# Performance work log

Measured on AMD Instinct MI355X. Metric: run time of the kernel, lower is better.

## Reference

```python
import jax, jax.numpy as jnp
import numpy as np


def setup_inputs() -> dict:
    key = jax.random.key(0)
    ks = jax.random.split(key, 6)
    B, S, D = 2, 2048, 1024
    E, DFF = 8, 2048  # E includes always-on expert 0; router sees E-1 routed experts
    scale = 0.02
    return {
        "hidden_states": jax.random.normal(ks[0], (B, S, D), dtype=jnp.float32),
        "router_w": jax.random.normal(ks[1], (D, E - 1), dtype=jnp.float32) * scale,
        "router_b": jnp.zeros((E - 1,), dtype=jnp.float32),
        "wg": jax.random.normal(ks[2], (E, D, DFF), dtype=jnp.float32) * scale,
        "wu": jax.random.normal(ks[3], (E, D, DFF), dtype=jnp.float32) * scale,
        "wd": jax.random.normal(ks[4], (E, DFF, D), dtype=jnp.float32) * scale,
        "top_k": 2,
    }


def _expert_mlp(x, wg_e, wu_e, wd_e):
    # SwiGLU MLP: down( silu(x @ gate) * (x @ up) )
    return (jax.nn.silu(x @ wg_e) * (x @ wu_e)) @ wd_e


def reference(hidden_states, router_w, router_b, wg, wu, wd, top_k):
    B, S, D = hidden_states.shape
    E = wg.shape[0]  # total experts incl. always-on expert 0
    x = hidden_states.reshape(-1, D)  # [T, D]
    T = x.shape[0]

    # Router over E-1 routed experts, softmax in float32
    router_logits = x @ router_w + router_b  # [T, E-1]
    probs = jax.nn.softmax(router_logits.astype(jnp.float32), axis=-1)
    topw, topi = jax.lax.top_k(probs, top_k)  # [T, k]
    topw = topw / jnp.sum(topw, axis=-1, keepdims=True)
    topw = topw.astype(x.dtype)

    # Dense combine weights over routed experts (0 for unselected)
    cw = jnp.zeros((T, E - 1), dtype=x.dtype)
    cw = cw.at[jnp.arange(T)[:, None], topi].add(topw)  # [T, E-1]

    # Always-on expert 0 with weight 1
    out = _expert_mlp(x, wg[0], wu[0], wd[0])  # [T, D]

    # Routed experts 1..E-1 (static small loop over experts)
    for e in range(1, E):
        ye = _expert_mlp(x, wg[e], wu[e], wd[e])  # [T, D]
        out = out + cw[:, e - 1, None] * ye

    return out.reshape(B, S, -1)
```

## Files before the change

kernel.cpp:

```cpp
#include <hip/hip_runtime.h>

#define T_TOK 4096
#define DIM   1024
#define DFF   2048
#define NE    8
#define NR    7
#define MAXNB 71
#define NY    (32 + MAXNB)

typedef __bf16 bf16x8 __attribute__((ext_vector_type(8)));
typedef float  floatx4 __attribute__((ext_vector_type(4)));

__device__ __forceinline__ unsigned short f32_bf16(float f) {
  union { float f; unsigned int u; } v; v.f = f;
  unsigned int u = v.u;
  unsigned int r = (u + 0x7FFFu + ((u >> 16) & 1u)) >> 16;
  return (unsigned short)r;
}

typedef __attribute__((address_space(3))) void lds_void_t;
typedef const __attribute__((address_space(1))) void g_void_t;

__device__ __forceinline__ void gld16(const void* g, void* l) {
  __builtin_amdgcn_global_load_lds((g_void_t*)g, (lds_void_t*)l, 16, 0, 0);
}

__global__ __launch_bounds__(256) void cvt_x_kernel(const float4* __restrict__ in,
                                                    ushort4* __restrict__ out) {
  int i = blockIdx.x * 256 + threadIdx.x;
  float4 v = in[i];
  ushort4 o;
  o.x = f32_bf16(v.x); o.y = f32_bf16(v.y);
  o.z = f32_bf16(v.z); o.w = f32_bf16(v.w);
  out[i] = o;
}

__global__ __launch_bounds__(256) void router_kernel(const float* __restrict__ x,
                                                     const float* __restrict__ rw,
                                                     const float* __restrict__ rb,
                                                     int* __restrict__ idxR,
                                                     float* __restrict__ wslR,
                                                     int* __restrict__ cnt,
                                                     int4* __restrict__ tokE,
                                                     float2* __restrict__ tokW) {
  const int lane = threadIdx.x & 63;
  const int t = blockIdx.x * 4 + (threadIdx.x >> 6);
  const float* xr = x + (size_t)t * DIM;
  float acc[NR];
#pragma unroll
  for (int e = 0; e < NR; e++) acc[e] = 0.f;
  for (int d = lane; d < DIM; d += 64) {
    float xv = xr[d];
#pragma unroll
    for (int e = 0; e < NR; e++) acc[e] += xv * rw[d * NR + e];
  }
#pragma unroll
  for (int off = 32; off > 0; off >>= 1) {
#pragma unroll
    for (int e = 0; e < NR; e++) acc[e] += __shfl_xor(acc[e], off, 64);
  }
  if (lane == 0) {
    float lg[NR];
    float m = -1e30f;
#pragma unroll
    for (int e = 0; e < NR; e++) { lg[e] = acc[e] + rb[e]; m = fmaxf(m, lg[e]); }
    float p[NR], s = 0.f;
#pragma unroll
    for (int e = 0; e < NR; e++) { p[e] = expf(lg[e] - m); s += p[e]; }
#pragma unroll
    for (int e = 0; e < NR; e++) p[e] /= s;
    int i1 = 0;
#pragma unroll
    for (int e = 1; e < NR; e++) if (p[e] > p[i1]) i1 = e;
    int i2 = (i1 == 0) ? 1 : 0;
#pragma unroll
    for (int e = 0; e < NR; e++) if (e != i1 && p[e] > p[i2]) i2 = e;
    float w1 = p[i1], w2 = p[i2], sw = w1 + w2;
    float w1n = w1 / sw, w2n = w2 / sw;
    int s1 = atomicAdd(&cnt[i1], 1);
    idxR[i1 * 4096 + s1] = t; wslR[i1 * 4096 + s1] = w1n;
    int s2 = atomicAdd(&cnt[i2], 1);
    idxR[i2 * 4096 + s2] = t; wslR[i2 * 4096 + s2] = w2n;
    int4 te; te.x = i1; te.y = s1; te.z = i2; te.w = s2;
    tokE[t] = te;
    float2 tw; tw.x = w1n; tw.y = w2n;
    tokW[t] = tw;
  }
}

__global__ __launch_bounds__(256) void sched_kernel(const int* __restrict__ cnt,
                                                    int* __restrict__ idxR,
                                                    float* __restrict__ wslR,
                                                    int4* __restrict__ schedAll,
                                                    int4* __restrict__ schedP,
                                                    int* __restrict__ prefOut,
                                                    int rsb) {
  __shared__ int nb[NR], pref[NR];
  if (threadIdx.x == 0) {
    int p = 0;
    for (int e = 0; e < NR; e++) { int c = cnt[e]; int n = (c + 127) >> 7; nb[e] = n; pref[e] = p; p += n; }
  }
  __syncthreads();
  if (threadIdx.x < NR) prefOut[threadIdx.x] = pref[threadIdx.x];
  for (int e = 0; e < NR; e++) {
    int c = cnt[e], top = nb[e] * 128;
    for (int i = c + (int)threadIdx.x; i < top; i += 256) {
      idxR[e * 4096 + i] = 0; wslR[e * 4096 + i] = 0.f;
    }
  }
  const int NBtot = pref[NR - 1] + nb[NR - 1];
  for (int y = threadIdx.x; y < 32; y += 256) {
    int4 ent; ent.x = 0; ent.y = -1; ent.z = y * 128; ent.w = 0;
    schedAll[y] = ent;
  }
  for (int y = threadIdx.x; y < MAXNB; y += 256) {
    int4 ent; ent.x = -1; ent.y = 0; ent.z = 0; ent.w = 0;
    if (y < NBtot) {
#pragma unroll
      for (int e = 0; e < NR; e++)
        if (y >= pref[e] && y < pref[e] + nb[e]) {
          int rb2 = y - pref[e];
          ent.x = e + 1; ent.y = e * 4096 + rb2 * 128; ent.z = rsb + y * 128;
        }
    }
    schedAll[32 + y] = ent;
  }
  for (int i = threadIdx.x; i < NR * 32; i += 256) {
    int e = i >> 5, rb2 = i & 31;
    int4 ent; ent.w = 0;
    if (rb2 < nb[e]) { ent.x = e + 1; ent.y = e * 4096 + rb2 * 128; ent.z = rb2 * 128; }
    else             { ent.x = -1; ent.y = 0; ent.z = 0; }
    schedP[i] = ent;
  }
}

__global__ __launch_bounds__(256) void transpose_cvt_kernel(
    const float* __restrict__ wg, const float* __restrict__ wu, const float* __restrict__ wd,
    unsigned short* __restrict__ wgt, unsigned short* __restrict__ wut,
    unsigned short* __restrict__ wdt) {
  __shared__ float tile[64][33];
  const int z = blockIdx.z;
  const float* src; unsigned short* dst; int R, C;
  if (z < 8)       { src = wg + (size_t)z * DIM * DFF;        dst = wgt + (size_t)z * DIM * DFF;        R = DIM; C = DFF; }
  else if (z < 16) { src = wu + (size_t)(z - 8) * DIM * DFF;  dst = wut + (size_t)(z - 8) * DIM * DFF;  R = DIM; C = DFF; }
  else             { src = wd + (size_t)(z - 16) * DFF * DIM; dst = wdt + (size_t)(z - 16) * DFF * DIM; R = DFF; C = DIM; }
  const int c0 = blockIdx.x * 32, r0 = blockIdx.y * 64;
  if (c0 >= C || r0 >= R) return;
  const int tx = threadIdx.x & 31, ty = threadIdx.x >> 5;
#pragma unroll
  for (int j = ty; j < 64; j += 8)
    tile[j][tx] = src[(size_t)(r0 + j) * C + c0 + tx];
  __syncthreads();
#pragma unroll
  for (int j = ty; j < 32; j += 8) {
    unsigned int lo = f32_bf16(tile[2 * tx][j]);
    unsigned int hi = f32_bf16(tile[2 * tx + 1][j]);
    *(unsigned int*)(dst + (size_t)(c0 + j) * R + r0 + 2 * tx) = lo | (hi << 16);
  }
}

__global__ __launch_bounds__(256, 2) void gemm1_kernel(
    const unsigned short* __restrict__ xb, const unsigned short* __restrict__ wgt,
    const unsigned short* __restrict__ wut, const int* __restrict__ idxR,
    const int4* __restrict__ sched, unsigned short* __restrict__ h) {
  const int4 ent = sched[blockIdx.y];
  if (ent.x < 0) return;
  __shared__ unsigned short As[128 * 32];
  __shared__ unsigned short Bg[128 * 32];
  __shared__ unsigned short Bu[128 * 32];
  const int tid = threadIdx.x, lane = tid & 63, wid = tid >> 6;
  const int n0 = blockIdx.x * 128;
  const int wm = (wid >> 1) * 64, wn = (wid & 1) * 64;
  floatx4 accg[4][4], accu[4][4];
  const floatx4 z4 = {0.f, 0.f, 0.f, 0.f};
#pragma unroll
  for (int i = 0; i < 4; i++)
#pragma unroll
    for (int j = 0; j < 4; j++) { accg[i][j] = z4; accu[i][j] = z4; }
  const unsigned short* wgt_e = wgt + (size_t)ent.x * DIM * DFF;
  const unsigned short* wut_e = wut + (size_t)ent.x * DIM * DFF;
  const int srow = tid >> 2, scol = (tid & 3) * 8;
  int tok0, tok1;
  if (ent.y < 0) { tok0 = ent.z + srow; tok1 = ent.z + srow + 64; }
  else           { tok0 = idxR[ent.y + srow]; tok1 = idxR[ent.y + srow + 64]; }
  const unsigned short* ap0 = xb + (size_t)tok0 * DIM + scol;
  const unsigned short* ap1 = xb + (size_t)tok1 * DIM + scol;
  const unsigned short* bg0 = wgt_e + (size_t)(n0 + srow) * DIM + scol;
  const unsigned short* bg1 = bg0 + (size_t)64 * DIM;
  const unsigned short* bu0 = wut_e + (size_t)(n0 + srow) * DIM + scol;
  const unsigned short* bu1 = bu0 + (size_t)64 * DIM;
  unsigned short* as0 = As + tid * 8;
  unsigned short* as1 = As + (256 + tid) * 8;
  unsigned short* bgl0 = Bg + tid * 8;
  unsigned short* bgl1 = Bg + (256 + tid) * 8;
  unsigned short* bul0 = Bu + tid * 8;
  unsigned short* bul1 = Bu + (256 + tid) * 8;
  const int fr = lane & 15, kq = (lane >> 4) * 8;
  for (int k0 = 0; k0 < DIM; k0 += 32) {
    __syncthreads();
    gld16(ap0 + k0, as0); gld16(ap1 + k0, as1);
    gld16(bg0 + k0, bgl0); gld16(bg1 + k0, bgl1);
    gld16(bu0 + k0, bul0); gld16(bu1 + k0, bul1);
    __syncthreads();
    bf16x8 af[4], bgf[4], buf2[4];
#pragma unroll
    for (int mi = 0; mi < 4; mi++) af[mi] = *(const bf16x8*)(As + (wm + mi * 16 + fr) * 32 + kq);
#pragma unroll
    for (int ni = 0; ni < 4; ni++) {
      bgf[ni]  = *(const bf16x8*)(Bg + (wn + ni * 16 + fr) * 32 + kq);
      buf2[ni] = *(const bf16x8*)(Bu + (wn + ni * 16 + fr) * 32 + kq);
    }
#pragma unroll
    for (int mi = 0; mi < 4; mi++)
#pragma unroll
      for (int ni = 0; ni < 4; ni++) {
        accg[mi][ni] = __builtin_amdgcn_mfma_f32_16x16x32_bf16(af[mi], bgf[ni], accg[mi][ni], 0, 0, 0);
        accu[mi][ni] = __builtin_amdgcn_mfma_f32_16x16x32_bf16(af[mi], buf2[ni], accu[mi][ni], 0, 0, 0);
      }
  }
  const int rb0 = wm + (lane >> 4) * 4;
  const int cb0 = n0 + wn + fr;
#pragma unroll
  for (int mi = 0; mi < 4; mi++)
#pragma unroll
    for (int ni = 0; ni < 4; ni++)
#pragma unroll
      for (int r = 0; r < 4; r++) {
        int lrow = rb0 + mi * 16 + r;
        int col = cb0 + ni * 16;
        float g = accg[mi][ni][r], u = accu[mi][ni][r];
        float hv = (g / (1.f + __expf(-g))) * u;
        h[(size_t)(ent.z + lrow) * DFF + col] = f32_bf16(hv);
      }
}

__global__ __launch_bounds__(256) void gemm2_kernel(
    const unsigned short* __restrict__ h, const unsigned short* __restrict__ wdt,
    const int4* __restrict__ sched, float* __restrict__ y) {
  const int4 ent = sched[blockIdx.y];
  if (ent.x < 0) return;
  __shared__ unsigned short As[128 * 32];
  __shared__ unsigned short Bs[128 * 32];
  const int tid = threadIdx.x, lane = tid & 63, wid = tid >> 6;
  const int n0 = blockIdx.x * 128;
  const int wm = (wid >> 1) * 64, wn = (wid & 1) * 64;
  floatx4 acc[4][4];
  const floatx4 z4 = {0.f, 0.f, 0.f, 0.f};
#pragma unroll
  for (int i = 0; i < 4; i++)
#pragma unroll
    for (int j = 0; j < 4; j++) acc[i][j] = z4;
  const unsigned short* wdt_e = wdt + (size_t)ent.x * DFF * DIM;
  const int srow = tid >> 2, scol = (tid & 3) * 8;
  const unsigned short* ap0 = h + (size_t)(ent.z + srow) * DFF + scol;
  const unsigned short* ap1 = ap0 + (size_t)64 * DFF;
  const unsigned short* bp0 = wdt_e + (size_t)(n0 + srow) * DFF + scol;
  const unsigned short* bp1 = bp0 + (size_t)64 * DFF;
  unsigned short* as0 = As + tid * 8;
  unsigned short* as1 = As + (256 + tid) * 8;
  unsigned short* bs0 = Bs + tid * 8;
  unsigned short* bs1 = Bs + (256 + tid) * 8;
  const int fr = lane & 15, kq = (lane >> 4) * 8;
  for (int k0 = 0; k0 < DFF; k0 += 32) {
    __syncthreads();
    gld16(ap0 + k0, as0); gld16(ap1 + k0, as1);
    gld16(bp0 + k0, bs0); gld16(bp1 + k0, bs1);
    __syncthreads();
    bf16x8 af[4], bf[4];
#pragma unroll
    for (int mi = 0; mi < 4; mi++) af[mi] = *(const bf16x8*)(As + (wm + mi * 16 + fr) * 32 + kq);
#pragma unroll
    for (int ni = 0; ni < 4; ni++) bf[ni] = *(const bf16x8*)(Bs + (wn + ni * 16 + fr) * 32 + kq);
#pragma unroll
    for (int mi = 0; mi < 4; mi++)
#pragma unroll
      for (int ni = 0; ni < 4; ni++)
        acc[mi][ni] = __builtin_amdgcn_mfma_f32_16x16x32_bf16(af[mi], bf[ni], acc[mi][ni], 0, 0, 0);
  }
  const int rb0 = wm + (lane >> 4) * 4;
  const int cb0 = n0 + wn + fr;
#pragma unroll
  for (int mi = 0; mi < 4; mi++)
#pragma unroll
    for (int ni = 0; ni < 4; ni++)
#pragma unroll
      for (int r = 0; r < 4; r++) {
        int lrow = rb0 + mi * 16 + r;
        y[(size_t)(ent.z + lrow) * DIM + cb0 + ni * 16] = acc[mi][ni][r];
      }
}

__global__ __launch_bounds__(256) void gemm2_atomic_kernel(
    const unsigned short* __restrict__ h, const unsigned short* __restrict__ wdt,
    const int* __restrict__ idxR, const float* __restrict__ wslR,
    const int4* __restrict__ sched, float* __restrict__ out) {
  const int4 ent = sched[blockIdx.y];
  if (ent.x < 0) return;
  __shared__ unsigned short As[128 * 32];
  __shared__ unsigned short Bs[128 * 32];
  const int tid = threadIdx.x, lane = tid & 63, wid = tid >> 6;
  const int n0 = blockIdx.x * 128;
  const int wm = (wid >> 1) * 64, wn = (wid & 1) * 64;
  floatx4 acc[4][4];
  const floatx4 z4 = {0.f, 0.f, 0.f, 0.f};
#pragma unroll
  for (int i = 0; i < 4; i++)
#pragma unroll
    for (int j = 0; j < 4; j++) acc[i][j] = z4;
  const unsigned short* wdt_e = wdt + (size_t)ent.x * DFF * DIM;
  const int srow = tid >> 2, scol = (tid & 3) * 8;
  const unsigned short* ap0 = h + (size_t)(ent.z + srow) * DFF + scol;
  const unsigned short* ap1 = ap0 + (size_t)64 * DFF;
  const unsigned short* bp0 = wdt_e + (size_t)(n0 + srow) * DFF + scol;
  const unsigned short* bp1 = bp0 + (size_t)64 * DFF;
  unsigned short* as0 = As + tid * 8;
  unsigned short* as1 = As + (256 + tid) * 8;
  unsigned short* bs0 = Bs + tid * 8;
  unsigned short* bs1 = Bs + (256 + tid) * 8;
  const int fr = lane & 15, kq = (lane >> 4) * 8;
  for (int k0 = 0; k0 < DFF; k0 += 32) {
    __syncthreads();
    gld16(ap0 + k0, as0); gld16(ap1 + k0, as1);
    gld16(bp0 + k0, bs0); gld16(bp1 + k0, bs1);
    __syncthreads();
    bf16x8 af[4], bf[4];
#pragma unroll
    for (int mi = 0; mi < 4; mi++) af[mi] = *(const bf16x8*)(As + (wm + mi * 16 + fr) * 32 + kq);
#pragma unroll
    for (int ni = 0; ni < 4; ni++) bf[ni] = *(const bf16x8*)(Bs + (wn + ni * 16 + fr) * 32 + kq);
#pragma unroll
    for (int mi = 0; mi < 4; mi++)
#pragma unroll
      for (int ni = 0; ni < 4; ni++)
        acc[mi][ni] = __builtin_amdgcn_mfma_f32_16x16x32_bf16(af[mi], bf[ni], acc[mi][ni], 0, 0, 0);
  }
  const int rb0 = wm + (lane >> 4) * 4;
  const int cb0 = n0 + wn + fr;
#pragma unroll
  for (int mi = 0; mi < 4; mi++)
#pragma unroll
    for (int r = 0; r < 4; r++) {
      int lrow = rb0 + mi * 16 + r;
      if (ent.y < 0) {
        int tok = ent.z + lrow;
#pragma unroll
        for (int ni = 0; ni < 4; ni++)
          out[(size_t)tok * DIM + cb0 + ni * 16] = acc[mi][ni][r];
      } else {
        int tok = idxR[ent.y + lrow];
        float s = wslR[ent.y + lrow];
        if (s != 0.f) {
#pragma unroll
          for (int ni = 0; ni < 4; ni++)
            atomicAdd(&out[(size_t)tok * DIM + cb0 + ni * 16], s * acc[mi][ni][r]);
        }
      }
    }
}

__global__ __launch_bounds__(256) void combine_kernel(const float* __restrict__ y,
                                                      const int4* __restrict__ tokE,
                                                      const float2* __restrict__ tokW,
                                                      const int* __restrict__ pref,
                                                      float* __restrict__ out) {
  const int t = blockIdx.x;
  const int c = threadIdx.x * 4;
  int4 te = tokE[t];
  float2 tw = tokW[t];
  int p1 = 4096 + pref[te.x] * 128 + te.y;
  int p2 = 4096 + pref[te.z] * 128 + te.w;
  float4 a = *(const float4*)(y + (size_t)t * DIM + c);
  float4 b = *(const float4*)(y + (size_t)p1 * DIM + c);
  float4 d = *(const float4*)(y + (size_t)p2 * DIM + c);
  float4 o;
  o.x = a.x + tw.x * b.x + tw.y * d.x;
  o.y = a.y + tw.x * b.y + tw.y * d.y;
  o.z = a.z + tw.x * b.z + tw.y * d.z;
  o.w = a.w + tw.x * b.w + tw.y * d.w;
  *(float4*)(out + (size_t)t * DIM + c) = o;
}

extern "C" void kernel_launch(void* const* d_in, const int* in_sizes, int n_in,
                              void* d_out, int out_size, void* d_ws, size_t ws_size,
                              hipStream_t stream) {
  const float* x  = (const float*)d_in[0];
  const float* rw = (const float*)d_in[1];
  const float* rb = (const float*)d_in[2];
  const float* wg = (const float*)d_in[3];
  const float* wu = (const float*)d_in[4];
  const float* wd = (const float*)d_in[5];
  float* out = (float*)d_out;

  const bool modeA = ws_size >= (size_t)163300000;
  const bool modeB = !modeA && ws_size >= (size_t)146700000;
  const size_t H_ROWS = modeA ? 13184 : (modeB ? 9088 : 4096);
  const int rsb = modeA ? 4096 : 0;

  char* p = (char*)d_ws;
  unsigned short* xb  = (unsigned short*)p; p += (size_t)T_TOK * DIM * 2;
  unsigned short* h   = (unsigned short*)p; p += H_ROWS * DFF * 2;
  unsigned short* wgt = (unsigned short*)p;
  float*          y   = (float*)p;          p += (size_t)NE * DIM * DFF * 2;
  unsigned short* wut = (unsigned short*)p; p += (size_t)NE * DIM * DFF * 2;
  unsigned short* wdt = (unsigned short*)p; p += (size_t)NE * DIM * DFF * 2;
  int*   idxR = (int*)p;   p += (size_t)NR * 4096 * 4;
  float* wslR;
  if (modeA) { wslR = (float*)wdt; }
  else       { wslR = (float*)p; p += (size_t)NR * 4096 * 4; }
  int*   cnt  = (int*)p;      p += 64;
  int*   pref = (int*)p;      p += 64;
  int4*  schedAll = (int4*)p; p += 2048;
  int4*  schedP   = (int4*)p; p += 4096;
  int4*  tokE = (int4*)p;     p += (size_t)T_TOK * 16;
  float2* tokW = (float2*)p;  p += (size_t)T_TOK * 8;

  cvt_x_kernel<<<dim3(T_TOK * DIM / 4 / 256), 256, 0, stream>>>((const float4*)x, (ushort4*)xb);
  hipMemsetAsync(cnt, 0, 64, stream);
  router_kernel<<<dim3(T_TOK / 4), 256, 0, stream>>>(x, rw, rb, idxR, wslR, cnt, tokE, tokW);
  sched_kernel<<<dim3(1), 256, 0, stream>>>(cnt, idxR, wslR, schedAll, schedP, pref, rsb);
  transpose_cvt_kernel<<<dim3(64, 32, 24), 256, 0, stream>>>(wg, wu, wd, wgt, wut, wdt);

  if (modeA) {
    gemm1_kernel<<<dim3(DFF / 128, NY), 256, 0, stream>>>(xb, wgt, wut, idxR, schedAll, h);
    gemm2_kernel<<<dim3(DIM / 128, NY), 256, 0, stream>>>(h, wdt, schedAll, y);
    combine_kernel<<<dim3(T_TOK), 256, 0, stream>>>(y, tokE, tokW, pref, out);
  } else if (modeB) {
    gemm1_kernel<<<dim3(DFF / 128, 32), 256, 0, stream>>>(xb, wgt, wut, idxR, schedAll, h);
    gemm2_atomic_kernel<<<dim3(DIM / 128, 32), 256, 0, stream>>>(h, wdt, idxR, wslR, schedAll, out);
    gemm1_kernel<<<dim3(DFF / 128, MAXNB), 256, 0, stream>>>(xb, wgt, wut, idxR, schedAll + 32, h);
    gemm2_atomic_kernel<<<dim3(DIM / 128, MAXNB), 256, 0, stream>>>(h, wdt, idxR, wslR, schedAll + 32, out);
  } else {
    gemm1_kernel<<<dim3(DFF / 128, 32), 256, 0, stream>>>(xb, wgt, wut, idxR, schedAll, h);
    gemm2_atomic_kernel<<<dim3(DIM / 128, 32), 256, 0, stream>>>(h, wdt, idxR, wslR, schedAll, out);
    for (int e = 0; e < NR; e++) {
      gemm1_kernel<<<dim3(DFF / 128, 32), 256, 0, stream>>>(xb, wgt, wut, idxR, schedP + e * 32, h);
      gemm2_atomic_kernel<<<dim3(DIM / 128, 32), 256, 0, stream>>>(h, wdt, idxR, wslR, schedP + e * 32, out);
    }
  }
}
```

Before: 594.2 us.

## Rewrite grouped GEMMs with 512-thread triple-buffered pipeline, swizzled LDS, XCD remap

Both expert GEMM kernels move to 512-thread blocks with K-tile 64 and a three-stage LDS ring buffer. Global-to-LDS prefetch of the stage two tiles ahead is interleaved between MFMA phases using s_barrier, sched_barrier and setprio. LDS rows are XOR-swizzled to avoid bank conflicts, and the 1D grid is remapped so that neighbouring tiles land on the same XCD for better L2 reuse. gemm2 also widens its N tile to 256. The aim is to hide memory latency and raise MFMA utilization, at the cost of more LDS per block (144KB), which may limit occupancy.

```diff
diff --git a/kernel.cpp b/kernel.cpp
--- a/kernel.cpp
+++ b/kernel.cpp
@@ -159,135 +159,284 @@
   }
 }
 
-__global__ __launch_bounds__(256, 2) void gemm1_kernel(
+__global__ __launch_bounds__(512, 2) void gemm1_kernel(
     const unsigned short* __restrict__ xb, const unsigned short* __restrict__ wgt,
     const unsigned short* __restrict__ wut, const int* __restrict__ idxR,
-    const int4* __restrict__ sched, unsigned short* __restrict__ h) {
-  const int4 ent = sched[blockIdx.y];
+    const int4* __restrict__ sched, unsigned short* __restrict__ h, int gx) {
+  const int nblk = gridDim.x;
+  int bid = blockIdx.x;
+  { int q = nblk >> 3, r = nblk & 7, xc = bid & 7, p = bid >> 3;
+    bid = (xc < r ? xc * (q + 1) : r * (q + 1) + (xc - r) * q) + p; }
+  const int by = bid / gx, bx = bid - by * gx;
+  const int4 ent = sched[by];
   if (ent.x < 0) return;
-  __shared__ unsigned short As[128 * 32];
-  __shared__ unsigned short Bg[128 * 32];
-  __shared__ unsigned short Bu[128 * 32];
+  __shared__ unsigned short smem[3 * 24576];
   const int tid = threadIdx.x, lane = tid & 63, wid = tid >> 6;
-  const int n0 = blockIdx.x * 128;
-  const int wm = (wid >> 1) * 64, wn = (wid & 1) * 64;
-  floatx4 accg[4][4], accu[4][4];
-  const floatx4 z4 = {0.f, 0.f, 0.f, 0.f};
-#pragma unroll
-  for (int i = 0; i < 4; i++)
-#pragma unroll
-    for (int j = 0; j < 4; j++) { accg[i][j] = z4; accu[i][j] = z4; }
+  const int n0 = bx * 128;
+  const int wm64 = (wid >> 2) * 64, wn32 = (wid & 3) * 32;
+  const int fr = lane & 15, kq8 = lane >> 4, x7 = fr & 7;
+  const int r0 = tid >> 3;
+  const int c8 = ((tid & 7) ^ (r0 & 7)) * 8;
+  int tok0, tok1;
+  if (ent.y < 0) { tok0 = ent.z + r0; tok1 = ent.z + r0 + 64; }
+  else           { tok0 = idxR[ent.y + r0]; tok1 = idxR[ent.y + r0 + 64]; }
   const unsigned short* wgt_e = wgt + (size_t)ent.x * DIM * DFF;
   const unsigned short* wut_e = wut + (size_t)ent.x * DIM * DFF;
-  const int srow = tid >> 2, scol = (tid & 3) * 8;
-  int tok0, tok1;
-  if (ent.y < 0) { tok0 = ent.z + srow; tok1 = ent.z + srow + 64; }
-  else           { tok0 = idxR[ent.y + srow]; tok1 = idxR[ent.y + srow + 64]; }
-  const unsigned short* ap0 = xb + (size_t)tok0 * DIM + scol;
-  const unsigned short* ap1 = xb + (size_t)tok1 * DIM + scol;
-  const unsigned short* bg0 = wgt_e + (size_t)(n0 + srow) * DIM + scol;
-  const unsigned short* bg1 = bg0 + (size_t)64 * DIM;
-  const unsigned short* bu0 = wut_e + (size_t)(n0 + srow) * DIM + scol;
-  const unsigned short* bu1 = bu0 + (size_t)64 * DIM;
-  unsigned short* as0 = As + tid * 8;
-  unsigned short* as1 = As + (256 + tid) * 8;
-  unsigned short* bgl0 = Bg + tid * 8;
-  unsigned short* bgl1 = Bg + (256 + tid) * 8;
-  unsigned short* bul0 = Bu + tid * 8;
-  unsigned short* bul1 = Bu + (256 + tid) * 8;
-  const int fr = lane & 15, kq = (lane >> 4) * 8;
-  for (int k0 = 0; k0 < DIM; k0 += 32) {
-    __syncthreads();
-    gld16(ap0 + k0, as0); gld16(ap1 + k0, as1);
-    gld16(bg0 + k0, bgl0); gld16(bg1 + k0, bgl1);
-    gld16(bu0 + k0, bul0); gld16(bu1 + k0, bul1);
-    __syncthreads();
-    bf16x8 af[4], bgf[4], buf2[4];
-#pragma unroll
-    for (int mi = 0; mi < 4; mi++) af[mi] = *(const bf16x8*)(As + (wm + mi * 16 + fr) * 32 + kq);
-#pragma unroll
-    for (int ni = 0; ni < 4; ni++) {
-      bgf[ni]  = *(const bf16x8*)(Bg + (wn + ni * 16 + fr) * 32 + kq);
-      buf2[ni] = *(const bf16x8*)(Bu + (wn + ni * 16 + fr) * 32 + kq);
-    }
-#pragma unroll
-    for (int mi = 0; mi < 4; mi++)
-#pragma unroll
-      for (int ni = 0; ni < 4; ni++) {
-        accg[mi][ni] = __builtin_amdgcn_mfma_f32_16x16x32_bf16(af[mi], bgf[ni], accg[mi][ni], 0, 0, 0);
-        accu[mi][ni] = __builtin_amdgcn_mfma_f32_16x16x32_bf16(af[mi], buf2[ni], accu[mi][ni], 0, 0, 0);
-      }
-  }
-  const int rb0 = wm + (lane >> 4) * 4;
-  const int cb0 = n0 + wn + fr;
+  const unsigned short* gA0 = xb + (size_t)tok0 * DIM + c8;
+  const unsigned short* gA1 = xb + (size_t)tok1 * DIM + c8;
+  const unsigned short* gG0 = wgt_e + (size_t)(n0 + r0) * DIM + c8;
+  const unsigned short* gG1 = gG0 + (size_t)64 * DIM;
+  const unsigned short* gU0 = wut_e + (size_t)(n0 + r0) * DIM + c8;
+  const unsigned short* gU1 = gU0 + (size_t)64 * DIM;
+  int offA[2][2], offB[2][2];
+#pragma unroll
+  for (int mi = 0; mi < 2; mi++)
+#pragma unroll
+    for (int kk = 0; kk < 2; kk++)
+      offA[mi][kk] = (wm64 + mi * 16 + fr) * 64 + (((kk * 4 + kq8) ^ x7) * 8);
+#pragma unroll
+  for (int ni = 0; ni < 2; ni++)
+#pragma unroll
+    for (int kk = 0; kk < 2; kk++)
+      offB[ni][kk] = (wn32 + ni * 16 + fr) * 64 + (((kk * 4 + kq8) ^ x7) * 8);
+  floatx4 accg[4][2], accu[4][2];
+  const floatx4 z4 = {0.f, 0.f, 0.f, 0.f};
+#pragma unroll
+  for (int i = 0; i < 4; i++)
+#pragma unroll
+    for (int j = 0; j < 2; j++) { accg[i][j] = z4; accu[i][j] = z4; }
+  {
+    unsigned short* d = smem + tid * 8;
+    gld16(gA0, d);             gld16(gA1, d + 4096);
+    gld16(gG0, d + 8192);      gld16(gG1, d + 12288);
+    gld16(gU0, d + 16384);     gld16(gU1, d + 20480);
+    unsigned short* e = smem + 24576 + tid * 8;
+    gld16(gA0 + 64, e);        gld16(gA1 + 64, e + 4096);
+    gld16(gG0 + 64, e + 8192); gld16(gG1 + 64, e + 12288);
+    gld16(gU0 + 64, e + 16384); gld16(gU1 + 64, e + 20480);
+  }
+  asm volatile("s_waitcnt vmcnt(6)" ::: "memory");
+  __builtin_amdgcn_s_barrier();
+  int b = 0;
+  for (int k = 0; k < 16; ++k) {
+    const unsigned short* Bb = smem + b * 24576;
+    int b2 = b + 2; if (b2 >= 3) b2 -= 3;
+    unsigned short* db2 = smem + b2 * 24576 + tid * 8;
+    const bool pf = (k < 14);
+    const int kt = (k + 2) * 64;
+    bf16x8 a[2][2], bg[2][2], bu[2][2];
+#pragma unroll
+    for (int mi = 0; mi < 2; mi++)
+#pragma unroll
+      for (int kk = 0; kk < 2; kk++) a[mi][kk] = *(const bf16x8*)(Bb + offA[mi][kk]);
+#pragma unroll
+    for (int ni = 0; ni < 2; ni++)
+#pragma unroll
+      for (int kk = 0; kk < 2; kk++) bg[ni][kk] = *(const bf16x8*)(Bb + 8192 + offB[ni][kk]);
+    if (pf) { gld16(gA0 + kt, db2); gld16(gA1 + kt, db2 + 4096); }
+    __builtin_amdgcn_sched_barrier(0);
+    __builtin_amdgcn_s_barrier();
+    __builtin_amdgcn_s_setprio(1);
+#pragma unroll
+    for (int mi = 0; mi < 2; mi++)
+#pragma unroll
+      for (int ni = 0; ni < 2; ni++)
+#pragma unroll
+        for (int kk = 0; kk < 2; kk++)
+          accg[mi][ni] = __builtin_amdgcn_mfma_f32_16x16x32_bf16(a[mi][kk], bg[ni][kk], accg[mi][ni], 0, 0, 0);
+    __builtin_amdgcn_s_setprio(0);
+    __builtin_amdgcn_sched_barrier(0);
+    __builtin_amdgcn_s_barrier();
+#pragma unroll
+    for (int ni = 0; ni < 2; ni++)
+#pragma unroll
+      for (int kk = 0; kk < 2; kk++) bu[ni][kk] = *(const bf16x8*)(Bb + 16384 + offB[ni][kk]);
+    if (pf) { gld16(gG0 + kt, db2 + 8192); gld16(gG1 + kt, db2 + 12288); }
+    __builtin_amdgcn_sched_barrier(0);
+    __builtin_amdgcn_s_barrier();
+    __builtin_amdgcn_s_setprio(1);
+#pragma unroll
+    for (int mi = 0; mi < 2; mi++)
+#pragma unroll
+      for (int ni = 0; ni < 2; ni++)
+#pragma unroll
+        for (int kk = 0; kk < 2; kk++)
+          accu[mi][ni] = __builtin_amdgcn_mfma_f32_16x16x32_bf16(a[mi][kk], bu[ni][kk], accu[mi][ni], 0, 0, 0);
+    __builtin_amdgcn_s_setprio(0);
+    __builtin_amdgcn_sched_barrier(0);
+    __builtin_amdgcn_s_barrier();
+#pragma unroll
+    for (int mi = 0; mi < 2; mi++)
+#pragma unroll
+      for (int kk = 0; kk < 2; kk++) a[mi][kk] = *(const bf16x8*)(Bb + 2048 + offA[mi][kk]);
+    if (pf) { gld16(gU0 + kt, db2 + 16384); gld16(gU1 + kt, db2 + 20480); }
+    __builtin_amdgcn_sched_barrier(0);
+    __builtin_amdgcn_s_barrier();
+    __builtin_amdgcn_s_setprio(1);
+#pragma unroll
+    for (int mi = 0; mi < 2; mi++)
+#pragma unroll
+      for (int ni = 0; ni < 2; ni++)
+#pragma unroll
+        for (int kk = 0; kk < 2; kk++) {
+          accg[2 + mi][ni] = __builtin_amdgcn_mfma_f32_16x16x32_bf16(a[mi][kk], bg[ni][kk], accg[2 + mi][ni], 0, 0, 0);
+          accu[2 + mi][ni] = __builtin_amdgcn_mfma_f32_16x16x32_bf16(a[mi][kk], bu[ni][kk], accu[2 + mi][ni], 0, 0, 0);
+        }
+    __builtin_amdgcn_s_setprio(0);
+    __builtin_amdgcn_sched_barrier(0);
+    if (k < 14)       asm volatile("s_waitcnt vmcnt(6)" ::: "memory");
+    else if (k == 14) asm volatile("s_waitcnt vmcnt(0)" ::: "memory");
+    __builtin_amdgcn_s_barrier();
+    b++; if (b == 3) b = 0;
+  }
+  const int rb = kq8 * 4;
 #pragma unroll
   for (int mi = 0; mi < 4; mi++)
 #pragma unroll
-    for (int ni = 0; ni < 4; ni++)
+    for (int ni = 0; ni < 2; ni++)
 #pragma unroll
       for (int r = 0; r < 4; r++) {
-        int lrow = rb0 + mi * 16 + r;
-        int col = cb0 + ni * 16;
+        int row = ent.z + wm64 + mi * 16 + rb + r;
+        int col = n0 + wn32 + ni * 16 + fr;
         float g = accg[mi][ni][r], u = accu[mi][ni][r];
         float hv = (g / (1.f + __expf(-g))) * u;
-        h[(size_t)(ent.z + lrow) * DFF + col] = f32_bf16(hv);
+        h[(size_t)row * DFF + col] = f32_bf16(hv);
       }
 }
 
-__global__ __launch_bounds__(256) void gemm2_kernel(
-    const unsigned short* __restrict__ h, const unsigned short* __restrict__ wdt,
-    const int4* __restrict__ sched, float* __restrict__ y) {
-  const int4 ent = sched[blockIdx.y];
+__global__ __launch_bounds__(512, 2) void gemm2_kernel(
+    const unsigned short* __restrict__ hsrc, const unsigned short* __restrict__ wdt,
+    const int4* __restrict__ sched, float* __restrict__ y, int gx) {
+  const int nblk = gridDim.x;
+  int bid = blockIdx.x;
+  { int q = nblk >> 3, r = nblk & 7, xc = bid & 7, p = bid >> 3;
+    bid = (xc < r ? xc * (q + 1) : r * (q + 1) + (xc - r) * q) + p; }
+  const int by = bid / gx, bx = bid - by * gx;
+  const int4 ent = sched[by];
   if (ent.x < 0) return;
-  __shared__ unsigned short As[128 * 32];
-  __shared__ unsigned short Bs[128 * 32];
+  __shared__ unsigned short smem[3 * 24576];
   const int tid = threadIdx.x, lane = tid & 63, wid = tid >> 6;
-  const int n0 = blockIdx.x * 128;
-  const int wm = (wid >> 1) * 64, wn = (wid & 1) * 64;
+  const int n0 = bx * 256;
+  const int wm64 = (wid >> 2) * 64, wn64 = (wid & 3) * 64;
+  const int fr = lane & 15, kq8 = lane >> 4, x7 = fr & 7;
+  const int r0 = tid >> 3;
+  const int c8 = ((tid & 7) ^ (r0 & 7)) * 8;
+  const unsigned short* wdt_e = wdt + (size_t)ent.x * DFF * DIM;
+  const unsigned short* gA0 = hsrc + (size_t)(ent.z + r0) * DFF + c8;
+  const unsigned short* gA1 = gA0 + (size_t)64 * DFF;
+  const unsigned short* gB0 = wdt_e + (size_t)(n0 + r0) * DFF + c8;
+  const unsigned short* gB1 = gB0 + (size_t)64 * DFF;
+  const unsigned short* gB2 = gB0 + (size_t)128 * DFF;
+  const unsigned short* gB3 = gB0 + (size_t)192 * DFF;
+  int offA[2][2], offB[2][2];
+#pragma unroll
+  for (int mi = 0; mi < 2; mi++)
+#pragma unroll
+    for (int kk = 0; kk < 2; kk++)
+      offA[mi][kk] = (wm64 + mi * 16 + fr) * 64 + (((kk * 4 + kq8) ^ x7) * 8);
+#pragma unroll
+  for (int ni = 0; ni < 2; ni++)
+#pragma unroll
+    for (int kk = 0; kk < 2; kk++)
+      offB[ni][kk] = (wn64 + ni * 16 + fr) * 64 + (((kk * 4 + kq8) ^ x7) * 8);
   floatx4 acc[4][4];
   const floatx4 z4 = {0.f, 0.f, 0.f, 0.f};
 #pragma unroll
   for (int i = 0; i < 4; i++)
 #pragma unroll
     for (int j = 0; j < 4; j++) acc[i][j] = z4;
-  const unsigned short* wdt_e = wdt + (size_t)ent.x * DFF * DIM;
-  const int srow = tid >> 2, scol = (tid & 3) * 8;
-  const unsigned short* ap0 = h + (size_t)(ent.z + srow) * DFF + scol;
-  const unsigned short* ap1 = ap0 + (size_t)64 * DFF;
-  const unsigned short* bp0 = wdt_e + (size_t)(n0 + srow) * DFF + scol;
-  const unsigned short* bp1 = bp0 + (size_t)64 * DFF;
-  unsigned short* as0 = As + tid * 8;
-  unsigned short* as1 = As + (256 + tid) * 8;
-  unsigned short* bs0 = Bs + tid * 8;
-  unsigned short* bs1 = Bs + (256 + tid) * 8;
-  const int fr = lane & 15, kq = (lane >> 4) * 8;
-  for (int k0 = 0; k0 < DFF; k0 += 32) {
-    __syncthreads();
-    gld16(ap0 + k0, as0); gld16(ap1 + k0, as1);
-    gld16(bp0 + k0, bs0); gld16(bp1 + k0, bs1);
-    __syncthreads();
-    bf16x8 af[4], bf[4];
-#pragma unroll
-    for (int mi = 0; mi < 4; mi++) af[mi] = *(const bf16x8*)(As + (wm + mi * 16 + fr) * 32 + kq);
-#pragma unroll
-    for (int ni = 0; ni < 4; ni++) bf[ni] = *(const bf16x8*)(Bs + (wn + ni * 16 + fr) * 32 + kq);
-#pragma unroll
-    for (int mi = 0; mi < 4; mi++)
-#pragma unroll
-      for (int ni = 0; ni < 4; ni++)
-        acc[mi][ni] = __builtin_amdgcn_mfma_f32_16x16x32_bf16(af[mi], bf[ni], acc[mi][ni], 0, 0, 0);
-  }
-  const int rb0 = wm + (lane >> 4) * 4;
-  const int cb0 = n0 + wn + fr;
+  {
+    unsigned short* d = smem + tid * 8;
+    gld16(gA0, d);             gld16(gA1, d + 4096);
+    gld16(gB0, d + 8192);      gld16(gB1, d + 12288);
+    gld16(gB2, d + 16384);     gld16(gB3, d + 20480);
+    unsigned short* e = smem + 24576 + tid * 8;
+    gld16(gA0 + 64, e);        gld16(gA1 + 64, e + 4096);
+    gld16(gB0 + 64, e + 8192); gld16(gB1 + 64, e + 12288);
+    gld16(gB2 + 64, e + 16384); gld16(gB3 + 64, e + 20480);
+  }
+  asm volatile("s_waitcnt vmcnt(6)" ::: "memory");
+  __builtin_amdgcn_s_barrier();
+  int b = 0;
+  for (int k = 0; k < 32; ++k) {
+    const unsigned short* Bb = smem + b * 24576;
+    int b2 = b + 2; if (b2 >= 3) b2 -= 3;
+    unsigned short* db2 = smem + b2 * 24576 + tid * 8;
+    const bool pf = (k < 30);
+    const int kt = (k + 2) * 64;
+    bf16x8 a[2][2], b0[2][2], b1[2][2];
+#pragma unroll
+    for (int mi = 0; mi < 2; mi++)
+#pragma unroll
+      for (int kk = 0; kk < 2; kk++) a[mi][kk] = *(const bf16x8*)(Bb + offA[mi][kk]);
+#pragma unroll
+    for (int ni = 0; ni < 2; ni++)
+#pragma unroll
+      for (int kk = 0; kk < 2; kk++) b0[ni][kk] = *(const bf16x8*)(Bb + 8192 + offB[ni][kk]);
+    if (pf) { gld16(gA0 + kt, db2); gld16(gA1 + kt, db2 + 4096); }
+    __builtin_amdgcn_sched_barrier(0);
+    __builtin_amdgcn_s_barrier();
+    __builtin_amdgcn_s_setprio(1);
+#pragma unroll
+    for (int mi = 0; mi < 2; mi++)
+#pragma unroll
+      for (int ni = 0; ni < 2; ni++)
+#pragma unroll
+        for (int kk = 0; kk < 2; kk++)
+          acc[mi][ni] = __builtin_amdgcn_mfma_f32_16x16x32_bf16(a[mi][kk], b0[ni][kk], acc[mi][ni], 0, 0, 0);
+    __builtin_amdgcn_s_setprio(0);
+    __builtin_amdgcn_sched_barrier(0);
+    __builtin_amdgcn_s_barrier();
+#pragma unroll
+    for (int ni = 0; ni < 2; ni++)
+#pragma unroll
+      for (int kk = 0; kk < 2; kk++) b1[ni][kk] = *(const bf16x8*)(Bb + 10240 + offB[ni][kk]);
+    if (pf) { gld16(gB0 + kt, db2 + 8192); gld16(gB1 + kt, db2 + 12288); }
+    __builtin_amdgcn_sched_barrier(0);
+    __builtin_amdgcn_s_barrier();
+    __builtin_amdgcn_s_setprio(1);
+#pragma unroll
+    for (int mi = 0; mi < 2; mi++)
+#pragma unroll
+      for (int ni = 0; ni < 2; ni++)
+#pragma unroll
+        for (int kk = 0; kk < 2; kk++)
+          acc[mi][2 + ni] = __builtin_amdgcn_mfma_f32_16x16x32_bf16(a[mi][kk], b1[ni][kk], acc[mi][2 + ni], 0, 0, 0);
+    __builtin_amdgcn_s_setprio(0);
+    __builtin_amdgcn_sched_barrier(0);
+    __builtin_amdgcn_s_barrier();
+#pragma unroll
+    for (int mi = 0; mi < 2; mi++)
+#pragma unroll
+      for (int kk = 0; kk < 2; kk++) a[mi][kk] = *(const bf16x8*)(Bb + 2048 + offA[mi][kk]);
+    if (pf) { gld16(gB2 + kt, db2 + 16384); gld16(gB3 + kt, db2 + 20480); }
+    __builtin_amdgcn_sched_barrier(0);
+    __builtin_amdgcn_s_barrier();
+    __builtin_amdgcn_s_setprio(1);
+#pragma unroll
+    for (int mi = 0; mi < 2; mi++)
+#pragma unroll
+      for (int ni = 0; ni < 2; ni++)
+#pragma unroll
+        for (int kk = 0; kk < 2; kk++) {
+          acc[2 + mi][ni]     = __builtin_amdgcn_mfma_f32_16x16x32_bf16(a[mi][kk], b0[ni][kk], acc[2 + mi][ni], 0, 0, 0);
+          acc[2 + mi][2 + ni] = __builtin_amdgcn_mfma_f32_16x16x32_bf16(a[mi][kk], b1[ni][kk], acc[2 + mi][2 + ni], 0, 0, 0);
+        }
+    __builtin_amdgcn_s_setprio(0);
+    __builtin_amdgcn_sched_barrier(0);
+    if (k < 30)       asm volatile("s_waitcnt vmcnt(6)" ::: "memory");
+    else if (k == 30) asm volatile("s_waitcnt vmcnt(0)" ::: "memory");
+    __builtin_amdgcn_s_barrier();
+    b++; if (b == 3) b = 0;
+  }
+  const int rb = kq8 * 4;
 #pragma unroll
   for (int mi = 0; mi < 4; mi++)
 #pragma unroll
     for (int ni = 0; ni < 4; ni++)
 #pragma unroll
-      for (int r = 0; r < 4; r++) {
-        int lrow = rb0 + mi * 16 + r;
-        y[(size_t)(ent.z + lrow) * DIM + cb0 + ni * 16] = acc[mi][ni][r];
-      }
+      for (int r = 0; r < 4; r++)
+        y[(size_t)(ent.z + wm64 + mi * 16 + rb + r) * DIM + n0 + wn64 + ni * 16 + fr] = acc[mi][ni][r];
 }
 
 __global__ __launch_bounds__(256) void gemm2_atomic_kernel(
@@ -421,19 +570,19 @@
   transpose_cvt_kernel<<<dim3(64, 32, 24), 256, 0, stream>>>(wg, wu, wd, wgt, wut, wdt);
 
   if (modeA) {
-    gemm1_kernel<<<dim3(DFF / 128, NY), 256, 0, stream>>>(xb, wgt, wut, idxR, schedAll, h);
-    gemm2_kernel<<<dim3(DIM / 128, NY), 256, 0, stream>>>(h, wdt, schedAll, y);
+    gemm1_kernel<<<dim3((DFF / 128) * NY), 512, 0, stream>>>(xb, wgt, wut, idxR, schedAll, h, DFF / 128);
+    gemm2_kernel<<<dim3((DIM / 256) * NY), 512, 0, stream>>>(h, wdt, schedAll, y, DIM / 256);
     combine_kernel<<<dim3(T_TOK), 256, 0, stream>>>(y, tokE, tokW, pref, out);
   } else if (modeB) {
-    gemm1_kernel<<<dim3(DFF / 128, 32), 256, 0, stream>>>(xb, wgt, wut, idxR, schedAll, h);
+    gemm1_kernel<<<dim3((DFF / 128) * 32), 512, 0, stream>>>(xb, wgt, wut, idxR, schedAll, h, DFF / 128);
     gemm2_atomic_kernel<<<dim3(DIM / 128, 32), 256, 0, stream>>>(h, wdt, idxR, wslR, schedAll, out);
-    gemm1_kernel<<<dim3(DFF / 128, MAXNB), 256, 0, stream>>>(xb, wgt, wut, idxR, schedAll + 32, h);
+    gemm1_kernel<<<dim3((DFF / 128) * MAXNB), 512, 0, stream>>>(xb, wgt, wut, idxR, schedAll + 32, h, DFF / 128);
     gemm2_atomic_kernel<<<dim3(DIM / 128, MAXNB), 256, 0, stream>>>(h, wdt, idxR, wslR, schedAll + 32, out);
   } else {
-    gemm1_kernel<<<dim3(DFF / 128, 32), 256, 0, stream>>>(xb, wgt, wut, idxR, schedAll, h);
+    gemm1_kernel<<<dim3((DFF / 128) * 32), 512, 0, stream>>>(xb, wgt, wut, idxR, schedAll, h, DFF / 128);
     gemm2_atomic_kernel<<<dim3(DIM / 128, 32), 256, 0, stream>>>(h, wdt, idxR, wslR, schedAll, out);
     for (int e = 0; e < NR; e++) {
-      gemm1_kernel<<<dim3(DFF / 128, 32), 256, 0, stream>>>(xb, wgt, wut, idxR, schedP + e * 32, h);
+      gemm1_kernel<<<dim3((DFF / 128) * 32), 512, 0, stream>>>(xb, wgt, wut, idxR, schedP + e * 32, h, DFF / 128);
       gemm2_atomic_kernel<<<dim3(DIM / 128, 32), 256, 0, stream>>>(h, wdt, idxR, wslR, schedP + e * 32, out);
     }
   }
```

Result: faster. 566.9 us (-4.6%).
